# Optimization experiments

Hardware: AMD Instinct MI355X
Metric: run time of the kernel (lower is better)

## Reference

```python
import jax, jax.numpy as jnp
import numpy as np

DT = 0.01
NLAG = 50           # int(maxlag / dt), maxlag = 0.5 s
NMA = 20
NC = 8192
NT = 4096


def _xcorr(data1, data2):
    # torch F.conv1d(data1.view(1, nc, nt), data2.view(nc, 1, nt),
    #                padding=NLAG+1, groups=nc)
    # == per-channel sliding cross-correlation.
    lhs = data1[None]            # (1, NC, NT)
    rhs = data2[:, None, :]      # (NC, 1, NT) -- one tiny filter per group
    out = jax.lax.conv_general_dilated(
        lhs, rhs,
        window_strides=(1,),
        padding=[(NLAG + 1, NLAG + 1)],
        dimension_numbers=("NCH", "OIH", "NCH"),
        feature_group_count=NC,
    )
    return out                   # (1, NC, L), L = 2*NLAG + 3 when nt1 == nt2


def _moving_average(x, nma=NMA):
    # Faithful to CCModel.moving_average: AvgPool1d(nma, stride=1, pad=nma//2)
    # applied after permute(0,2,1), i.e. the pooling runs over the CHANNEL
    # axis, with zero padding included in the mean (count_include_pad=True),
    # then sliced back to nc channels.
    nb, nc, L = x.shape
    pad = nma // 2
    xp = jnp.pad(x, ((0, 0), (pad, pad), (0, 0)))
    cs = jnp.concatenate(
        [jnp.zeros((nb, 1, L), x.dtype), jnp.cumsum(xp, axis=1)], axis=1)
    win = (cs[:, nma:, :] - cs[:, :-nma, :]) / nma   # sliding sum / nma
    return win[:, :nc, :]


def _pick_maxabs(R, dt):
    # pick_Rkt_maxabs: per-channel max-|cc| pick.
    L = R.shape[-1]
    nlag_c = (L - 1) // 2        # zero-lag index
    imax = jnp.argmax(jnp.abs(R), axis=-1)                              # (nb, nc)
    vmain = jnp.take_along_axis(R, imax[..., None], axis=-1)[..., 0]    # signed peak
    vpos = jnp.max(R, axis=-1)
    vneg = jnp.min(R, axis=-1)
    vside = jnp.where(vmain >= 0, vneg, vpos)        # opposite-sign extremum
    tmax = (imax - nlag_c).astype(R.dtype) * dt
    return vmain, vside, tmax


def setup_inputs() -> dict:
    key = jax.random.key(0)
    k1, k2, k3, k4 = jax.random.split(key, 4)
    data1 = jax.random.normal(k1, (NC, NT), dtype=jnp.float32)
    data2 = jax.random.normal(k2, (NC, NT), dtype=jnp.float32)
    event1 = jax.random.randint(k3, (1,), 0, 1000, dtype=jnp.int32)
    event2 = jax.random.randint(k4, (1,), 0, 1000, dtype=jnp.int32)
    return {"data1": data1, "data2": data2, "event1": event1, "event2": event2}


def reference(data1, data2, event1, event2):
    xcor = _xcorr(data1, data2)              # (1, NC, 2*NLAG+3)
    xcor = _moving_average(xcor, NMA)        # in-place overwrite in torch
    vmax, vmin, tmax = _pick_maxabs(xcor, DT)
    return xcor, vmax, vmin, tmax
```

## Files before the change

kernel.cpp:

```cpp
#include <hip/hip_runtime.h>

#define NC 8192
#define NT 4096
#define NLAGS 103
#define WS_STRIDE 104
#define XBASE (NC*NLAGS)

#define PADL 52
#define PADR 60
#define P32(x) ((x) + (((x) >> 5) << 2))
#define D1PA 4736
#define SMEMF (2*D1PA)
#define CPB 4
#define LPW 28
#define REDS 29

__global__ __launch_bounds__(256, 3)
void xcorr_kernel(const float* __restrict__ g1, const float* __restrict__ g2,
                  float* __restrict__ ws) {
    __shared__ __align__(16) float smem[SMEMF];
    const int tid  = threadIdx.x;
    const int wv   = tid >> 6;
    const int lane = tid & 63;
    const int c0   = blockIdx.x * CPB;

    #pragma unroll
    for (int bb = 0; bb < 2; ++bb) {
        float* buf = smem + bb * D1PA;
        if (tid < PADL) buf[P32(tid)] = 0.f;
        if (tid < PADR) buf[P32(PADL + NT + tid)] = 0.f;
    }
    {
        const float4* r = (const float4*)(g1 + (size_t)c0 * NT);
        #pragma unroll
        for (int i = 0; i < 4; ++i) {
            float4 v = r[tid + 256*i];
            int x = PADL + 4*(tid + 256*i);
            *(float4*)&smem[P32(x)] = v;
        }
    }
    __syncthreads();

    #pragma unroll 1
    for (int ci = 0; ci < CPB; ++ci) {
        const int c = c0 + ci;
        float* cur  = smem + (ci & 1) * D1PA;
        float* nxtb = smem + ((ci & 1) ^ 1) * D1PA;
        const float* g2c = g2 + (size_t)c * NT;

        float4 nx0, nx1, nx2, nx3;
        const bool hasnext = (ci + 1 < CPB);
        if (hasnext) {
            const float4* r = (const float4*)(g1 + (size_t)(c + 1) * NT);
            nx0 = r[tid]; nx1 = r[tid + 256]; nx2 = r[tid + 512]; nx3 = r[tid + 768];
        }

        float acc[LPW];
        #pragma unroll
        for (int l = 0; l < LPW; ++l) acc[l] = 0.f;

        #pragma unroll 1
        for (int it = 0; it < 2; ++it) {
            const int k0 = it*2048 + lane*32;
            float b[32];
            #pragma unroll
            for (int t = 0; t < 8; ++t) {
                float4 v = *(const float4*)(g2c + k0 + 4*t);
                b[4*t]=v.x; b[4*t+1]=v.y; b[4*t+2]=v.z; b[4*t+3]=v.w;
            }
            float w[60];
            const int wb = k0 + 28*wv;
            #pragma unroll
            for (int t = 0; t < 15; ++t) {
                float4 v = *(const float4*)&cur[P32(wb + 4*t)];
                w[4*t]=v.x; w[4*t+1]=v.y; w[4*t+2]=v.z; w[4*t+3]=v.w;
            }
            #pragma unroll
            for (int j = 0; j < 32; ++j)
                #pragma unroll
                for (int l = 0; l < LPW; ++l)
                    acc[l] = fmaf(w[l+j], b[j], acc[l]);
        }

        if (hasnext) {
            int x = PADL + 4*tid;
            *(float4*)&nxtb[P32(x)]        = nx0;
            *(float4*)&nxtb[P32(x + 1024)] = nx1;
            *(float4*)&nxtb[P32(x + 2048)] = nx2;
            *(float4*)&nxtb[P32(x + 3072)] = nx3;
        }
        __syncthreads();

        #pragma unroll
        for (int l = 0; l < LPW; ++l) acc[l] += __shfl_down(acc[l], 32);
        float* red = cur + wv * (32*REDS);
        if (lane < 32) {
            #pragma unroll
            for (int l = 0; l < LPW; ++l) red[lane*REDS + l] = acc[l];
        }
        if (lane < LPW) {
            float sum = 0.f;
            #pragma unroll
            for (int r = 0; r < 32; ++r) sum += red[r*REDS + lane];
            const int L = 28*wv - 1 + lane;
            if (L >= 0 && L < NLAGS) ws[(size_t)c * WS_STRIDE + L] = sum;
        }
        if (tid < PADL) cur[P32(tid)] = 0.f;
        __syncthreads();
    }
}

#define TS 112
__global__ __launch_bounds__(256, 4)
void ma_pick_kernel(const float* __restrict__ ws, float* __restrict__ out) {
    __shared__ float tile[52*TS];
    __shared__ float matile[32*TS];
    const int tid = threadIdx.x;
    const int c0  = blockIdx.x * 32;

    for (int i = tid; i < 52*TS; i += 256) {
        int r   = i / TS;
        int col = i - r*TS;
        int g   = c0 - 10 + r;
        float v = 0.f;
        if (g >= 0 && g < NC && col < NLAGS) v = ws[(size_t)g*WS_STRIDE + col];
        tile[i] = v;
    }
    __syncthreads();

    {
        const int l = tid & 127;
        const int h = tid >> 7;
        if (l < NLAGS) {
            const int cc0 = h * 16;
            float s = 0.f;
            #pragma unroll
            for (int r = 0; r < 20; ++r) s += tile[(cc0 + r)*TS + l];
            #pragma unroll 1
            for (int cc = cc0; cc < cc0 + 16; ++cc) {
                float ma = s / 20.0f;
                matile[cc*TS + l] = ma;
                out[(size_t)(c0 + cc)*NLAGS + l] = ma;
                s += tile[(cc + 20)*TS + l] - tile[cc*TS + l];
            }
        }
    }
    __syncthreads();

    const int wv = tid >> 6, lane = tid & 63;
    #pragma unroll 1
    for (int s8 = 0; s8 < 8; ++s8) {
        const int cc = wv*8 + s8;
        float v1 = matile[cc*TS + lane];
        float a1 = fabsf(v1);
        int   i1 = lane;
        float vmx = v1, vmn = v1;
        if (lane < NLAGS - 64) {
            float v2 = matile[cc*TS + 64 + lane];
            float a2 = fabsf(v2);
            vmx = fmaxf(vmx, v2); vmn = fminf(vmn, v2);
            if (a2 > a1) { a1 = a2; i1 = 64 + lane; v1 = v2; }
        }
        #pragma unroll
        for (int d = 32; d >= 1; d >>= 1) {
            float oa  = __shfl_xor(a1, d);
            int   oi  = __shfl_xor(i1, d);
            float ov  = __shfl_xor(v1, d);
            float omx = __shfl_xor(vmx, d);
            float omn = __shfl_xor(vmn, d);
            vmx = fmaxf(vmx, omx);
            vmn = fminf(vmn, omn);
            if (oa > a1 || (oa == a1 && oi < i1)) { a1 = oa; i1 = oi; v1 = ov; }
        }
        if (lane == 0) {
            const int ch = c0 + cc;
            out[XBASE + ch]        = v1;
            out[XBASE + NC + ch]   = (v1 >= 0.f) ? vmn : vmx;
            out[XBASE + 2*NC + ch] = (float)(i1 - 51) * 0.01f;
        }
    }
}

extern "C" void kernel_launch(void* const* d_in, const int* in_sizes, int n_in,
                              void* d_out, int out_size, void* d_ws, size_t ws_size,
                              hipStream_t stream) {
    const float* g1 = (const float*)d_in[0];
    const float* g2 = (const float*)d_in[1];
    float* out = (float*)d_out;
    float* ws  = (float*)d_ws;

    hipLaunchKernelGGL(xcorr_kernel, dim3(NC/CPB), dim3(256), 0, stream, g1, g2, ws);
    hipLaunchKernelGGL(ma_pick_kernel, dim3(NC/32), dim3(256), 0, stream, ws, out);
}
```

Measured before the change: 324.5 us.

## Prefetch data2 rows into registers and move reduction scratch to dedicated LDS

Unrolls the two half-row iterations. The next channel's first data2 half and the current channel's second half are loaded into registers ahead of the FMA work, with sched_barriers so the global loads overlap compute. The cross-wave reduction scratch moves to its own LDS region instead of reusing the current data1 buffer. This removes one __syncthreads per channel and the re-zeroing of the pad. In exchange it uses more registers and more shared memory, which may lower occupancy below the launch-bounds target of 3 blocks.

Result: slower. 545.9 us (+68.2%).

```diff
diff --git a/kernel.cpp b/kernel.cpp
--- a/kernel.cpp
+++ b/kernel.cpp
@@ -10,19 +10,22 @@
 #define PADR 60
 #define P32(x) ((x) + (((x) >> 5) << 2))
 #define D1PA 4736
-#define SMEMF (2*D1PA)
 #define CPB 4
 #define LPW 28
 #define REDS 29
+#define REDF (4*32*REDS)
+#define SMEMF (2*D1PA + REDF)
 
 __global__ __launch_bounds__(256, 3)
 void xcorr_kernel(const float* __restrict__ g1, const float* __restrict__ g2,
                   float* __restrict__ ws) {
     __shared__ __align__(16) float smem[SMEMF];
+    float* red_all = smem + 2*D1PA;
     const int tid  = threadIdx.x;
     const int wv   = tid >> 6;
     const int lane = tid & 63;
     const int c0   = blockIdx.x * CPB;
+    const int klane = lane * 32;
 
     #pragma unroll
     for (int bb = 0; bb < 2; ++bb) {
@@ -32,48 +35,58 @@
     }
     {
         const float4* r = (const float4*)(g1 + (size_t)c0 * NT);
-        #pragma unroll
-        for (int i = 0; i < 4; ++i) {
-            float4 v = r[tid + 256*i];
-            int x = PADL + 4*(tid + 256*i);
-            *(float4*)&smem[P32(x)] = v;
-        }
+        float4 v0 = r[tid], v1 = r[tid+256], v2 = r[tid+512], v3 = r[tid+768];
+        const int x = PADL + 4*tid;
+        *(float4*)&smem[P32(x)]        = v0;
+        *(float4*)&smem[P32(x + 1024)] = v1;
+        *(float4*)&smem[P32(x + 2048)] = v2;
+        *(float4*)&smem[P32(x + 3072)] = v3;
     }
     __syncthreads();
+
+    float4 B0[8];
+    {
+        const float* p = g2 + (size_t)c0 * NT + klane;
+        #pragma unroll
+        for (int t = 0; t < 8; ++t) B0[t] = *(const float4*)(p + 4*t);
+    }
 
     #pragma unroll 1
     for (int ci = 0; ci < CPB; ++ci) {
         const int c = c0 + ci;
         float* cur  = smem + (ci & 1) * D1PA;
         float* nxtb = smem + ((ci & 1) ^ 1) * D1PA;
-        const float* g2c = g2 + (size_t)c * NT;
-
-        float4 nx0, nx1, nx2, nx3;
         const bool hasnext = (ci + 1 < CPB);
+
+        float4 NX0, NX1, NX2, NX3;
         if (hasnext) {
             const float4* r = (const float4*)(g1 + (size_t)(c + 1) * NT);
-            nx0 = r[tid]; nx1 = r[tid + 256]; nx2 = r[tid + 512]; nx3 = r[tid + 768];
-        }
+            NX0 = r[tid]; NX1 = r[tid+256]; NX2 = r[tid+512]; NX3 = r[tid+768];
+        }
+        float4 B1[8];
+        {
+            const float* p = g2 + (size_t)c * NT + 2048 + klane;
+            #pragma unroll
+            for (int t = 0; t < 8; ++t) B1[t] = *(const float4*)(p + 4*t);
+        }
+        __builtin_amdgcn_sched_barrier(0);
 
         float acc[LPW];
         #pragma unroll
         for (int l = 0; l < LPW; ++l) acc[l] = 0.f;
 
-        #pragma unroll 1
-        for (int it = 0; it < 2; ++it) {
-            const int k0 = it*2048 + lane*32;
+        {
+            const int ab = klane + 28*wv;
+            float w[60];
+            #pragma unroll
+            for (int t = 0; t < 15; ++t) {
+                float4 v = *(const float4*)&cur[P32(ab + 4*t)];
+                w[4*t]=v.x; w[4*t+1]=v.y; w[4*t+2]=v.z; w[4*t+3]=v.w;
+            }
             float b[32];
             #pragma unroll
             for (int t = 0; t < 8; ++t) {
-                float4 v = *(const float4*)(g2c + k0 + 4*t);
-                b[4*t]=v.x; b[4*t+1]=v.y; b[4*t+2]=v.z; b[4*t+3]=v.w;
-            }
-            float w[60];
-            const int wb = k0 + 28*wv;
-            #pragma unroll
-            for (int t = 0; t < 15; ++t) {
-                float4 v = *(const float4*)&cur[P32(wb + 4*t)];
-                w[4*t]=v.x; w[4*t+1]=v.y; w[4*t+2]=v.z; w[4*t+3]=v.w;
+                b[4*t]=B0[t].x; b[4*t+1]=B0[t].y; b[4*t+2]=B0[t].z; b[4*t+3]=B0[t].w;
             }
             #pragma unroll
             for (int j = 0; j < 32; ++j)
@@ -83,29 +96,51 @@
         }
 
         if (hasnext) {
-            int x = PADL + 4*tid;
-            *(float4*)&nxtb[P32(x)]        = nx0;
-            *(float4*)&nxtb[P32(x + 1024)] = nx1;
-            *(float4*)&nxtb[P32(x + 2048)] = nx2;
-            *(float4*)&nxtb[P32(x + 3072)] = nx3;
-        }
-        __syncthreads();
+            const int x = PADL + 4*tid;
+            *(float4*)&nxtb[P32(x)]        = NX0;
+            *(float4*)&nxtb[P32(x + 1024)] = NX1;
+            *(float4*)&nxtb[P32(x + 2048)] = NX2;
+            *(float4*)&nxtb[P32(x + 3072)] = NX3;
+            const float* p = g2 + (size_t)(c + 1) * NT + klane;
+            #pragma unroll
+            for (int t = 0; t < 8; ++t) B0[t] = *(const float4*)(p + 4*t);
+            __builtin_amdgcn_sched_barrier(0);
+        }
+
+        {
+            const int ab = 2048 + klane + 28*wv;
+            float w[60];
+            #pragma unroll
+            for (int t = 0; t < 15; ++t) {
+                float4 v = *(const float4*)&cur[P32(ab + 4*t)];
+                w[4*t]=v.x; w[4*t+1]=v.y; w[4*t+2]=v.z; w[4*t+3]=v.w;
+            }
+            float b[32];
+            #pragma unroll
+            for (int t = 0; t < 8; ++t) {
+                b[4*t]=B1[t].x; b[4*t+1]=B1[t].y; b[4*t+2]=B1[t].z; b[4*t+3]=B1[t].w;
+            }
+            #pragma unroll
+            for (int j = 0; j < 32; ++j)
+                #pragma unroll
+                for (int l = 0; l < LPW; ++l)
+                    acc[l] = fmaf(w[l+j], b[j], acc[l]);
+        }
 
         #pragma unroll
         for (int l = 0; l < LPW; ++l) acc[l] += __shfl_down(acc[l], 32);
-        float* red = cur + wv * (32*REDS);
+        float* red = red_all + wv * (32*REDS);
         if (lane < 32) {
             #pragma unroll
             for (int l = 0; l < LPW; ++l) red[lane*REDS + l] = acc[l];
         }
         if (lane < LPW) {
-            float sum = 0.f;
-            #pragma unroll
-            for (int r = 0; r < 32; ++r) sum += red[r*REDS + lane];
-            const int L = 28*wv - 1 + lane;
-            if (L >= 0 && L < NLAGS) ws[(size_t)c * WS_STRIDE + L] = sum;
-        }
-        if (tid < PADL) cur[P32(tid)] = 0.f;
+            float s = 0.f;
+            #pragma unroll
+            for (int r = 0; r < 32; ++r) s += red[r*REDS + lane];
+            const int L = 28*wv + lane - 1;
+            if (L >= 0 && L < NLAGS) ws[(size_t)c * WS_STRIDE + L] = s;
+        }
         __syncthreads();
     }
 }
```

## Stage data2 into LDS via async global_load_lds with XOR swizzle, one channel per block

Applied to the files above, without the earlier changes.

Each block now handles a single channel instead of four, dropping the manual double-buffered prefetch of the next data1 row. data2 is staged into shared memory with global_load_lds direct-to-LDS loads, and both data1 and data2 are read through XOR-swizzled addressing instead of the padded layout, to cut bank conflicts and global-load latency. Occupancy target rises from 3 to 4 blocks per CU. The cost is losing the cross-channel overlap of data1 loads with compute, and more blocks, each with its own setup and synchronisation overhead.

Result: faster. 314.7 us (-3.0%).

```diff
diff --git a/kernel.cpp b/kernel.cpp
--- a/kernel.cpp
+++ b/kernel.cpp
@@ -6,107 +6,99 @@
 #define WS_STRIDE 104
 #define XBASE (NC*NLAGS)
 
-#define PADL 52
-#define PADR 60
-#define P32(x) ((x) + (((x) >> 5) << 2))
-#define D1PA 4736
-#define SMEMF (2*D1PA)
-#define CPB 4
-#define LPW 28
-#define REDS 29
+#define D1LOG 4208
+#define D1DW  4224
+#define D2DW  4096
+#define REDS  29
+#define SMEMF (D1DW + D2DW)
 
-__global__ __launch_bounds__(256, 3)
+__device__ __forceinline__ int swz(int b) {
+    return b ^ (((b >> 7) & 7) << 4);
+}
+
+__global__ __launch_bounds__(256, 4)
 void xcorr_kernel(const float* __restrict__ g1, const float* __restrict__ g2,
                   float* __restrict__ ws) {
-    __shared__ __align__(16) float smem[SMEMF];
+    __shared__ __align__(128) float smem[SMEMF];
+    char* d1b = (char*)smem;
+    char* d2b = (char*)(smem + D1DW);
     const int tid  = threadIdx.x;
     const int wv   = tid >> 6;
     const int lane = tid & 63;
-    const int c0   = blockIdx.x * CPB;
+    const int c    = blockIdx.x;
+    const float* g1c = g1 + (size_t)c * NT;
+    const float* g2c = g2 + (size_t)c * NT;
 
     #pragma unroll
-    for (int bb = 0; bb < 2; ++bb) {
-        float* buf = smem + bb * D1PA;
-        if (tid < PADL) buf[P32(tid)] = 0.f;
-        if (tid < PADR) buf[P32(PADL + NT + tid)] = 0.f;
+    for (int t = 0; t < 4; ++t) {
+        const int O = 4096*wv + 1024*t + 16*lane;
+        const int S = O ^ ((lane >> 3) << 4);
+        __builtin_amdgcn_global_load_lds(
+            (const float*)((const char*)g2c + S),
+            (float*)(d2b + 4096*wv + 1024*t),
+            16, 0, 0);
     }
+
     {
-        const float4* r = (const float4*)(g1 + (size_t)c0 * NT);
-        #pragma unroll
-        for (int i = 0; i < 4; ++i) {
-            float4 v = r[tid + 256*i];
-            int x = PADL + 4*(tid + 256*i);
-            *(float4*)&smem[P32(x)] = v;
-        }
+        const float4* r = (const float4*)g1c;
+        float4 v0 = r[tid], v1 = r[tid+256], v2 = r[tid+512], v3 = r[tid+768];
+        if (tid < 52) *(float*)(d1b + swz(4*tid)) = 0.f;
+        if (tid < 60) *(float*)(d1b + swz(4*(4148 + tid))) = 0.f;
+        const int B = 208 + 16*tid;
+        *(float4*)(d1b + swz(B))         = v0;
+        *(float4*)(d1b + swz(B + 4096))  = v1;
+        *(float4*)(d1b + swz(B + 8192))  = v2;
+        *(float4*)(d1b + swz(B + 12288)) = v3;
     }
     __syncthreads();
 
+    float acc[28];
+    #pragma unroll
+    for (int l = 0; l < 28; ++l) acc[l] = 0.f;
+
     #pragma unroll 1
-    for (int ci = 0; ci < CPB; ++ci) {
-        const int c = c0 + ci;
-        float* cur  = smem + (ci & 1) * D1PA;
-        float* nxtb = smem + ((ci & 1) ^ 1) * D1PA;
-        const float* g2c = g2 + (size_t)c * NT;
-
-        float4 nx0, nx1, nx2, nx3;
-        const bool hasnext = (ci + 1 < CPB);
-        if (hasnext) {
-            const float4* r = (const float4*)(g1 + (size_t)(c + 1) * NT);
-            nx0 = r[tid]; nx1 = r[tid + 256]; nx2 = r[tid + 512]; nx3 = r[tid + 768];
-        }
-
-        float acc[LPW];
-        #pragma unroll
-        for (int l = 0; l < LPW; ++l) acc[l] = 0.f;
-
-        #pragma unroll 1
-        for (int it = 0; it < 2; ++it) {
-            const int k0 = it*2048 + lane*32;
-            float b[32];
+    for (int it = 0; it < 2; ++it) {
+        const int k0 = 2048*it + 32*lane;
+        float b[32];
+        {
+            const int base = 128*lane + 8192*it;
+            const int sx   = (lane & 7) << 4;
             #pragma unroll
             for (int t = 0; t < 8; ++t) {
-                float4 v = *(const float4*)(g2c + k0 + 4*t);
+                float4 v = *(const float4*)(d2b + ((base + 16*t) ^ sx));
                 b[4*t]=v.x; b[4*t+1]=v.y; b[4*t+2]=v.z; b[4*t+3]=v.w;
             }
-            float w[60];
-            const int wb = k0 + 28*wv;
+        }
+        float w[60];
+        {
+            const int xb = 4*(k0 + 28*wv);
             #pragma unroll
             for (int t = 0; t < 15; ++t) {
-                float4 v = *(const float4*)&cur[P32(wb + 4*t)];
+                float4 v = *(const float4*)(d1b + swz(xb + 16*t));
                 w[4*t]=v.x; w[4*t+1]=v.y; w[4*t+2]=v.z; w[4*t+3]=v.w;
             }
+        }
+        #pragma unroll
+        for (int j = 0; j < 32; ++j)
             #pragma unroll
-            for (int j = 0; j < 32; ++j)
-                #pragma unroll
-                for (int l = 0; l < LPW; ++l)
-                    acc[l] = fmaf(w[l+j], b[j], acc[l]);
-        }
+            for (int l = 0; l < 28; ++l)
+                acc[l] = fmaf(w[l+j], b[j], acc[l]);
+    }
 
-        if (hasnext) {
-            int x = PADL + 4*tid;
-            *(float4*)&nxtb[P32(x)]        = nx0;
-            *(float4*)&nxtb[P32(x + 1024)] = nx1;
-            *(float4*)&nxtb[P32(x + 2048)] = nx2;
-            *(float4*)&nxtb[P32(x + 3072)] = nx3;
-        }
-        __syncthreads();
-
+    __syncthreads();
+    #pragma unroll
+    for (int l = 0; l < 28; ++l) acc[l] += __shfl_down(acc[l], 32);
+    float* red = (float*)d2b + wv * (32*REDS);
+    if (lane < 32) {
         #pragma unroll
-        for (int l = 0; l < LPW; ++l) acc[l] += __shfl_down(acc[l], 32);
-        float* red = cur + wv * (32*REDS);
-        if (lane < 32) {
-            #pragma unroll
-            for (int l = 0; l < LPW; ++l) red[lane*REDS + l] = acc[l];
-        }
-        if (lane < LPW) {
-            float sum = 0.f;
-            #pragma unroll
-            for (int r = 0; r < 32; ++r) sum += red[r*REDS + lane];
-            const int L = 28*wv - 1 + lane;
-            if (L >= 0 && L < NLAGS) ws[(size_t)c * WS_STRIDE + L] = sum;
-        }
-        if (tid < PADL) cur[P32(tid)] = 0.f;
-        __syncthreads();
+        for (int l = 0; l < 28; ++l) red[lane*REDS + l] = acc[l];
+    }
+    if (lane < 28) {
+        float s = 0.f;
+        #pragma unroll
+        for (int r = 0; r < 32; ++r) s += red[r*REDS + lane];
+        const int L = 28*wv + lane - 1;
+        if (L >= 0 && L < NLAGS) ws[(size_t)c * WS_STRIDE + L] = s;
     }
 }
 
@@ -189,6 +181,6 @@
     float* out = (float*)d_out;
     float* ws  = (float*)d_ws;
 
-    hipLaunchKernelGGL(xcorr_kernel, dim3(NC/CPB), dim3(256), 0, stream, g1, g2, ws);
+    hipLaunchKernelGGL(xcorr_kernel, dim3(NC), dim3(256), 0, stream, g1, g2, ws);
     hipLaunchKernelGGL(ma_pick_kernel, dim3(NC/32), dim3(256), 0, stream, ws, out);
 }
```
